# Kernel tuning notes

Hardware: AMD Instinct MI355X
Metric: run time of the kernel (lower is better)

## Reference

```python
import jax, jax.numpy as jnp
import numpy as np

CODEBOOK_SIZE = 8192
DIM = 256
B, T = 8, 4096


def setup_inputs() -> dict:
    key = jax.random.key(0)
    k1, k2, k3 = jax.random.split(key, 3)
    h = jax.random.normal(k1, (B, T, DIM), dtype=jnp.float32)
    mask = jax.random.randint(k2, (B, T), 0, 2).astype(bool)
    codebook = jax.random.normal(k3, (CODEBOOK_SIZE, DIM), dtype=jnp.float32) * 0.02
    return {"h": h, "mask": mask, "codebook": codebook}


def reference(h, mask, codebook):
    Bb, Tt, D = h.shape
    flat = h.reshape(-1, D)  # (N, D)
    # squared euclidean distances (N, K)
    h2 = jnp.sum(flat * flat, axis=-1, keepdims=True)
    c2 = jnp.sum(codebook * codebook, axis=-1)
    dist = h2 + c2 - 2.0 * flat @ codebook.T
    indices = jnp.argmin(dist, axis=-1)  # (N,)
    z = codebook[indices].reshape(Bb, Tt, D)
    m = mask.astype(h.dtype)[:, :, None]  # (B, T, 1)
    denom = jnp.sum(m) * D + 1e-8
    commit_loss = jnp.sum((h - jax.lax.stop_gradient(z)) ** 2 * m) / denom
    codebook_loss = jnp.sum((jax.lax.stop_gradient(h) - z) ** 2 * m) / denom
    z_q = h + jax.lax.stop_gradient(z - h)  # straight-through estimator
    return z_q, indices.reshape(Bb, Tt), commit_loss, codebook_loss
```

## Files before the change

kernel.cpp:

```cpp
#include <hip/hip_runtime.h>

#define NPTS   32768
#define DIM    256
#define KCODES 8192
#define TAU    1e-2f
#define NCAP   16384

typedef __attribute__((ext_vector_type(8))) short bf16x8;
typedef __attribute__((ext_vector_type(4))) float f32x4;

__device__ __forceinline__ unsigned short f2bf(float x) {
  unsigned u = __float_as_uint(x);
  unsigned r = (u + 0x7fffu + ((u >> 16) & 1u)) >> 16;
  return (unsigned short)r;
}

__global__ __launch_bounds__(256) void bf16_norms_kernel(
    const float* __restrict__ src, unsigned short* __restrict__ hi,
    float* __restrict__ norms, int* __restrict__ flagcnt) {
  if (flagcnt && blockIdx.x == 0 && threadIdx.x == 0) *flagcnt = 0;
  int row = blockIdx.x * 4 + (threadIdx.x >> 6);
  int lane = threadIdx.x & 63;
  float4 a = reinterpret_cast<const float4*>(src)[row * 64 + lane];
  ushort4 hq;
  hq.x = f2bf(a.x); hq.y = f2bf(a.y); hq.z = f2bf(a.z); hq.w = f2bf(a.w);
  reinterpret_cast<ushort4*>(hi)[row * 64 + lane] = hq;
  float sx = a.x * a.x, sy = a.y * a.y, sz = a.z * a.z, sw = a.w * a.w;
  double s = (double)sx + (double)sy + (double)sz + (double)sw;
#pragma unroll
  for (int m = 32; m; m >>= 1) s += __shfl_xor(s, m, 64);
  if (lane == 0) norms[row] = (float)s;
}

__global__ __launch_bounds__(256) void norms_kernel(const float* __restrict__ src,
                                                    float* __restrict__ dst) {
  int row = blockIdx.x * 4 + (threadIdx.x >> 6);
  int lane = threadIdx.x & 63;
  float4 a = reinterpret_cast<const float4*>(src)[row * 64 + lane];
  float sx = a.x * a.x, sy = a.y * a.y, sz = a.z * a.z, sw = a.w * a.w;
  double s = (double)sx + (double)sy + (double)sz + (double)sw;
#pragma unroll
  for (int m = 32; m; m >>= 1) s += __shfl_xor(s, m, 64);
  if (lane == 0) dst[row] = (float)s;
}

__global__ __launch_bounds__(512, 2) void mfma_argmin_kernel(
    const unsigned short* __restrict__ hh, const unsigned short* __restrict__ chh,
    const float* __restrict__ c2f,
    float* __restrict__ bv, int* __restrict__ bi, float* __restrict__ b2o) {
  __shared__ __align__(16) unsigned short Ps[8192], Cs[8192];
  __shared__ float tb1[128][4], tb2[128][4];
  __shared__ int ti1[128][4];
  const int t = threadIdx.x;
  const int lane = t & 63;
  const int wid = t >> 6;
  const int wrow = wid >> 2;
  const int cgroup = wid & 3;
  const int b = blockIdx.x;
  const int v = (b & 7) * 64 + (b >> 3);
  const int sblk = v >> 8, pblk = v & 255;
  const int p0 = pblk * 128;
  const int cbase = sblk * (KCODES / 2);

  const int strow = t >> 2, stc = t & 3;
  const int ssw = strow & 7;
  const int stbase = strow * 128;
  const int wd0 = stbase + (((stc * 2) ^ ssw) << 4);
  const int wd1 = stbase + (((stc * 2 + 1) ^ ssw) << 4);
  const char* hhc = (const char*)hh;
  const char* chc = (const char*)chh;
  const unsigned poffs = (unsigned)(p0 + strow) * 512u + (unsigned)(stc * 32);
  const unsigned cbb = (unsigned)(cbase + strow) * 512u + (unsigned)(stc * 32);

  const int flane = lane & 15, fch = lane >> 4;
  int coff[2][2];
#pragma unroll
  for (int cr = 0; cr < 2; ++cr) {
    int ar = cgroup * 32 + cr * 16 + flane;
#pragma unroll
    for (int kp = 0; kp < 2; ++kp)
      coff[cr][kp] = ar * 128 + (((kp * 4 + fch) ^ (ar & 7)) << 4);
  }
  int poff[4][2];
#pragma unroll
  for (int pc = 0; pc < 4; ++pc) {
    int br = wrow * 64 + pc * 16 + flane;
#pragma unroll
    for (int kp = 0; kp < 2; ++kp)
      poff[pc][kp] = br * 128 + (((kp * 4 + fch) ^ (br & 7)) << 4);
  }

  float rb1[4], rb2[4];
  int ri1[4];
#pragma unroll
  for (int pc = 0; pc < 4; ++pc) { rb1[pc] = 3.4e38f; rb2[pc] = 3.4e38f; ri1[pc] = 0; }

#pragma unroll 1
  for (int cc = 0; cc < 32; ++cc) {
    f32x4 acc[8];
#pragma unroll
    for (int q = 0; q < 8; ++q) acc[q] = (f32x4){0.f, 0.f, 0.f, 0.f};
    const unsigned ccc = cbb + (unsigned)cc * 65536u;

#pragma unroll
    for (int dd = 0; dd < 4; ++dd) {
      const unsigned kk = (unsigned)(dd * 128);
      uint4 pa = *(const uint4*)(hhc + poffs + kk);
      uint4 pb = *(const uint4*)(hhc + poffs + kk + 16);
      uint4 ca = *(const uint4*)(chc + ccc + kk);
      uint4 cb2 = *(const uint4*)(chc + ccc + kk + 16);
      __syncthreads();
      *(uint4*)((char*)Ps + wd0) = pa;
      *(uint4*)((char*)Ps + wd1) = pb;
      *(uint4*)((char*)Cs + wd0) = ca;
      *(uint4*)((char*)Cs + wd1) = cb2;
      __syncthreads();
      bf16x8 cf[2][2];
#pragma unroll
      for (int cr = 0; cr < 2; ++cr)
#pragma unroll
        for (int kp = 0; kp < 2; ++kp)
          cf[cr][kp] = *(const bf16x8*)((const char*)Cs + coff[cr][kp]);
#pragma unroll
      for (int pc = 0; pc < 4; ++pc) {
        bf16x8 p0f = *(const bf16x8*)((const char*)Ps + poff[pc][0]);
        bf16x8 p1f = *(const bf16x8*)((const char*)Ps + poff[pc][1]);
        acc[pc] = __builtin_amdgcn_mfma_f32_16x16x32_bf16(cf[0][0], p0f, acc[pc], 0, 0, 0);
        acc[pc] = __builtin_amdgcn_mfma_f32_16x16x32_bf16(cf[0][1], p1f, acc[pc], 0, 0, 0);
        acc[4 + pc] = __builtin_amdgcn_mfma_f32_16x16x32_bf16(cf[1][0], p0f, acc[4 + pc], 0, 0, 0);
        acc[4 + pc] = __builtin_amdgcn_mfma_f32_16x16x32_bf16(cf[1][1], p1f, acc[4 + pc], 0, 0, 0);
      }
    }
    const int code0 = cbase + cc * 128 + cgroup * 32 + fch * 4;
    float c2v[2][4];
#pragma unroll
    for (int cr = 0; cr < 2; ++cr)
#pragma unroll
      for (int r = 0; r < 4; ++r)
        c2v[cr][r] = c2f[code0 + cr * 16 + r];
#pragma unroll
    for (int pc = 0; pc < 4; ++pc) {
#pragma unroll
      for (int cr = 0; cr < 2; ++cr)
#pragma unroll
        for (int r = 0; r < 4; ++r) {
          float sv = fmaf(-2.f, acc[cr * 4 + pc][r], c2v[cr][r]);
          if (sv < rb1[pc]) { rb2[pc] = rb1[pc]; rb1[pc] = sv; ri1[pc] = code0 + cr * 16 + r; }
          else if (sv < rb2[pc]) rb2[pc] = sv;
        }
    }
  }
#pragma unroll
  for (int pc = 0; pc < 4; ++pc) {
    float b1 = rb1[pc], b2 = rb2[pc];
    int i1 = ri1[pc];
#pragma unroll
    for (int m = 16; m <= 32; m <<= 1) {
      float ob1 = __shfl_xor(b1, m, 64);
      int oi1 = __shfl_xor(i1, m, 64);
      float ob2 = __shfl_xor(b2, m, 64);
      float loser = fmaxf(b1, ob1);
      float nb2 = fminf(fminf(b2, ob2), loser);
      if (ob1 < b1 || (ob1 == b1 && oi1 < i1)) { b1 = ob1; i1 = oi1; }
      b2 = nb2;
    }
    if (fch == 0) {
      int pl = wrow * 64 + pc * 16 + flane;
      tb1[pl][cgroup] = b1;
      ti1[pl][cgroup] = i1;
      tb2[pl][cgroup] = b2;
    }
  }
  __syncthreads();
  if (t < 128) {
    float b1 = tb1[t][0], b2 = tb2[t][0];
    int i1 = ti1[t][0];
#pragma unroll
    for (int w = 1; w < 4; ++w) {
      float nb1 = tb1[t][w], nb2v = tb2[t][w];
      int ni1 = ti1[t][w];
      float loser = fmaxf(b1, nb1);
      float m2 = fminf(fminf(b2, nb2v), loser);
      if (nb1 < b1 || (nb1 == b1 && ni1 < i1)) { b1 = nb1; i1 = ni1; }
      b2 = m2;
    }
    int p = p0 + t;
    bv[sblk * NPTS + p] = b1;
    bi[sblk * NPTS + p] = i1;
    b2o[sblk * NPTS + p] = b2;
  }
}

__global__ __launch_bounds__(256) void merge_flag_kernel(
    const float* __restrict__ bv, const int* __restrict__ bi,
    const float* __restrict__ b2o, int* __restrict__ idx,
    float* __restrict__ out_idx_f, int* __restrict__ flagcnt,
    int* __restrict__ flaglist) {
  int p = blockIdx.x * 256 + threadIdx.x;
  float b1 = bv[p]; int i1 = bi[p]; float b2 = b2o[p];
  {
    float pb1 = bv[NPTS + p];
    int pi1 = bi[NPTS + p];
    float pb2 = b2o[NPTS + p];
    float loser = fmaxf(b1, pb1);
    float nb2 = fminf(fminf(b2, pb2), loser);
    if (pb1 < b1 || (pb1 == b1 && pi1 < i1)) { b1 = pb1; i1 = pi1; }
    b2 = nb2;
  }
  idx[p] = i1;
  out_idx_f[p] = (float)i1;
  if (b2 - b1 < TAU) { int s = atomicAdd(flagcnt, 1); flaglist[s] = p; }
}

__global__ __launch_bounds__(256) void compact_kernel(
    const float* __restrict__ h, const float* __restrict__ h2f,
    const int* __restrict__ flagcnt, const int* __restrict__ flaglist,
    float* __restrict__ hc, float* __restrict__ h2c) {
  int n0 = *flagcnt;
  int n = n0 > NCAP ? NCAP : n0;
  int npad = (n + 127) & ~127;
  for (int e = blockIdx.x; e < npad; e += gridDim.x) {
    if (e < n) {
      int p = flaglist[e];
      if (threadIdx.x < 64)
        reinterpret_cast<float4*>(hc + (size_t)e * DIM)[threadIdx.x] =
            reinterpret_cast<const float4*>(h + (size_t)p * DIM)[threadIdx.x];
      if (threadIdx.x == 0) h2c[e] = h2f[p];
    } else {
      if (threadIdx.x < 64)
        reinterpret_cast<float4*>(hc + (size_t)e * DIM)[threadIdx.x] =
            make_float4(0.f, 0.f, 0.f, 0.f);
      if (threadIdx.x == 0) h2c[e] = 0.f;
    }
  }
}

__global__ __launch_bounds__(512, 2) void refine_gemm_kernel(
    const float* __restrict__ hc, const float* __restrict__ cb,
    const float* __restrict__ h2c, const float* __restrict__ c2f,
    const int* __restrict__ flagcnt,
    float* __restrict__ bv16, int* __restrict__ bi16) {
  const int n0 = *flagcnt;
  const int n = n0 > NCAP ? NCAP : n0;
  const int slice = blockIdx.x & 15;
  const int pblk = blockIdx.x >> 4;
  if (pblk * 128 >= n) return;
  __shared__ float hs[16][132];
  __shared__ float cs[16][260];
  const int t = threadIdx.x;
  const int ct = t & 31;
  const int pt = t >> 5;
  const int p0 = pblk * 128;
  const int cbase = slice * 512;
  float best[8]; int besti[8]; float h2r[8];
#pragma unroll
  for (int i = 0; i < 8; ++i) {
    best[i] = 3.4e38f; besti[i] = 0;
    h2r[i] = h2c[p0 + pt * 4 + ((i >> 2) << 6) + (i & 3)];
  }
#pragma unroll 1
  for (int cc = 0; cc < 2; ++cc) {
    const int c0 = cbase + cc * 256;
    float dot[8][8];
#pragma unroll
    for (int i = 0; i < 8; ++i)
#pragma unroll
      for (int j = 0; j < 8; ++j) dot[i][j] = 0.f;
#pragma unroll 1
    for (int dd = 0; dd < DIM / 16; ++dd) {
      const int d0 = dd * 16;
      {
        int p = t >> 2, k4 = (t & 3) << 2;
        float4 w = *reinterpret_cast<const float4*>(hc + (size_t)(p0 + p) * DIM + d0 + k4);
        hs[k4 + 0][p] = w.x; hs[k4 + 1][p] = w.y;
        hs[k4 + 2][p] = w.z; hs[k4 + 3][p] = w.w;
      }
#pragma unroll
      for (int l = 0; l < 2; ++l) {
        int F = t + l * 512;
        int c = F >> 2, k4 = (F & 3) << 2;
        float4 w = *reinterpret_cast<const float4*>(cb + (size_t)(c0 + c) * DIM + d0 + k4);
        cs[k4 + 0][c] = w.x; cs[k4 + 1][c] = w.y;
        cs[k4 + 2][c] = w.z; cs[k4 + 3][c] = w.w;
      }
      __syncthreads();
#pragma unroll
      for (int k = 0; k < 16; ++k) {
        float hv[8], cv[8];
        *reinterpret_cast<float4*>(&hv[0]) = *reinterpret_cast<const float4*>(&hs[k][pt * 4]);
        *reinterpret_cast<float4*>(&hv[4]) = *reinterpret_cast<const float4*>(&hs[k][pt * 4 + 64]);
        *reinterpret_cast<float4*>(&cv[0]) = *reinterpret_cast<const float4*>(&cs[k][ct * 4]);
        *reinterpret_cast<float4*>(&cv[4]) = *reinterpret_cast<const float4*>(&cs[k][ct * 4 + 128]);
#pragma unroll
        for (int i = 0; i < 8; ++i)
#pragma unroll
          for (int j = 0; j < 8; ++j) dot[i][j] = fmaf(hv[i], cv[j], dot[i][j]);
      }
      __syncthreads();
    }
#pragma unroll
    for (int j = 0; j < 8; ++j) {
      int cl = c0 + (ct << 2) + ((j >> 2) << 7) + (j & 3);
      float cc2 = c2f[cl];
#pragma unroll
      for (int i = 0; i < 8; ++i) {
        float A = h2r[i] + cc2;
        float s = A - 2.0f * dot[i][j];
        if (s < best[i]) { best[i] = s; besti[i] = cl; }
      }
    }
  }
#pragma unroll
  for (int i = 0; i < 8; ++i) {
    float b1 = best[i]; int i1 = besti[i];
#pragma unroll
    for (int m = 16; m; m >>= 1) {
      float so = __shfl_xor(b1, m, 64);
      int io = __shfl_xor(i1, m, 64);
      if (so < b1 || (so == b1 && io < i1)) { b1 = so; i1 = io; }
    }
    if (ct == 0) {
      int p = p0 + pt * 4 + ((i >> 2) << 6) + (i & 3);
      bv16[slice * NCAP + p] = b1;
      bi16[slice * NCAP + p] = i1;
    }
  }
}

__global__ __launch_bounds__(256) void scatter_kernel(
    const float* __restrict__ bv16, const int* __restrict__ bi16,
    const int* __restrict__ flagcnt, const int* __restrict__ flaglist,
    int* __restrict__ idx, float* __restrict__ out_idx_f) {
  int n0 = *flagcnt;
  int n = n0 > NCAP ? NCAP : n0;
  int e = blockIdx.x * 256 + threadIdx.x;
  if (e >= n) return;
  float b1 = bv16[e];
  int i1 = bi16[e];
#pragma unroll
  for (int s = 1; s < 16; ++s) {
    float nb = bv16[s * NCAP + e];
    int ni = bi16[s * NCAP + e];
    if (nb < b1 || (nb == b1 && ni < i1)) { b1 = nb; i1 = ni; }
  }
  int p = flaglist[e];
  idx[p] = i1;
  out_idx_f[p] = (float)i1;
}

__global__ __launch_bounds__(256) void refine_left_kernel(
    const float* __restrict__ h, const float* __restrict__ cb,
    const float* __restrict__ h2f, const float* __restrict__ c2f,
    const int* __restrict__ flagcnt, const int* __restrict__ flaglist,
    int* __restrict__ idx, float* __restrict__ out_idx_f) {
  __shared__ float hrow[DIM];
  __shared__ float rb[256];
  __shared__ int ri[256];
  const int n = *flagcnt;
  for (int e = NCAP + blockIdx.x; e < n; e += gridDim.x) {
    const int p = flaglist[e];
    __syncthreads();
    if (threadIdx.x < DIM / 4)
      reinterpret_cast<float4*>(hrow)[threadIdx.x] =
          reinterpret_cast<const float4*>(h + (size_t)p * DIM)[threadIdx.x];
    __syncthreads();
    const float h2 = h2f[p];
    float b1 = 3.4e38f;
    int i1 = 0x7fffffff;
    for (int c = threadIdx.x; c < KCODES; c += 256) {
      const float4* crow = reinterpret_cast<const float4*>(cb + (size_t)c * DIM);
      float dot = 0.f;
#pragma unroll 16
      for (int d4 = 0; d4 < DIM / 4; ++d4) {
        float4 cv = crow[d4];
        dot = fmaf(hrow[4 * d4 + 0], cv.x, dot);
        dot = fmaf(hrow[4 * d4 + 1], cv.y, dot);
        dot = fmaf(hrow[4 * d4 + 2], cv.z, dot);
        dot = fmaf(hrow[4 * d4 + 3], cv.w, dot);
      }
      float A = h2 + c2f[c];
      float s = fmaf(-2.f, dot, A);
      if (s < b1) { b1 = s; i1 = c; }
    }
    rb[threadIdx.x] = b1;
    ri[threadIdx.x] = i1;
    __syncthreads();
    for (int step = 128; step; step >>= 1) {
      if (threadIdx.x < step) {
        float ob = rb[threadIdx.x + step];
        int oi = ri[threadIdx.x + step];
        if (ob < rb[threadIdx.x] || (ob == rb[threadIdx.x] && oi < ri[threadIdx.x])) {
          rb[threadIdx.x] = ob;
          ri[threadIdx.x] = oi;
        }
      }
      __syncthreads();
    }
    if (threadIdx.x == 0) { idx[p] = ri[0]; out_idx_f[p] = (float)ri[0]; }
  }
}

__global__ __launch_bounds__(512, 2) void argmin_fp32_kernel(
    const float* __restrict__ h, const float* __restrict__ cb,
    const float* __restrict__ h2f, const float* __restrict__ c2f,
    float* __restrict__ bestval, int* __restrict__ bestidx) {
  __shared__ float hs[16][132];
  __shared__ float cs[16][260];
  const int t = threadIdx.x;
  const int ct = t & 31;
  const int pt = t >> 5;
  const int b = blockIdx.x;
  const int v = (b & 7) * 64 + (b >> 3);
  const int sblk = v >> 8;
  const int pblk = v & 255;
  const int p0 = pblk * 128;
  const int cbase = sblk * (KCODES / 2);
  float best[8]; int besti[8]; float h2r[8];
#pragma unroll
  for (int i = 0; i < 8; ++i) {
    best[i] = 3.4e38f; besti[i] = 0;
    h2r[i] = h2f[p0 + pt * 4 + ((i >> 2) << 6) + (i & 3)];
  }
#pragma unroll 1
  for (int cc = 0; cc < (KCODES / 2) / 256; ++cc) {
    const int c0 = cbase + cc * 256;
    float dot[8][8];
#pragma unroll
    for (int i = 0; i < 8; ++i)
#pragma unroll
      for (int j = 0; j < 8; ++j) dot[i][j] = 0.f;
#pragma unroll 1
    for (int dd = 0; dd < DIM / 16; ++dd) {
      const int d0 = dd * 16;
      {
        int p = t >> 2, k4 = (t & 3) << 2;
        float4 w = *reinterpret_cast<const float4*>(h + (p0 + p) * DIM + d0 + k4);
        hs[k4 + 0][p] = w.x; hs[k4 + 1][p] = w.y;
        hs[k4 + 2][p] = w.z; hs[k4 + 3][p] = w.w;
      }
#pragma unroll
      for (int l = 0; l < 2; ++l) {
        int F = t + l * 512;
        int c = F >> 2, k4 = (F & 3) << 2;
        float4 w = *reinterpret_cast<const float4*>(cb + (c0 + c) * DIM + d0 + k4);
        cs[k4 + 0][c] = w.x; cs[k4 + 1][c] = w.y;
        cs[k4 + 2][c] = w.z; cs[k4 + 3][c] = w.w;
      }
      __syncthreads();
#pragma unroll
      for (int k = 0; k < 16; ++k) {
        float hv[8], cv[8];
        *reinterpret_cast<float4*>(&hv[0]) = *reinterpret_cast<const float4*>(&hs[k][pt * 4]);
        *reinterpret_cast<float4*>(&hv[4]) = *reinterpret_cast<const float4*>(&hs[k][pt * 4 + 64]);
        *reinterpret_cast<float4*>(&cv[0]) = *reinterpret_cast<const float4*>(&cs[k][ct * 4]);
        *reinterpret_cast<float4*>(&cv[4]) = *reinterpret_cast<const float4*>(&cs[k][ct * 4 + 128]);
#pragma unroll
        for (int i = 0; i < 8; ++i)
#pragma unroll
          for (int j = 0; j < 8; ++j) dot[i][j] = fmaf(hv[i], cv[j], dot[i][j]);
      }
      __syncthreads();
    }
#pragma unroll
    for (int j = 0; j < 8; ++j) {
      int cl = c0 + (ct << 2) + ((j >> 2) << 7) + (j & 3);
      float cc2 = c2f[cl];
#pragma unroll
      for (int i = 0; i < 8; ++i) {
        float A = h2r[i] + cc2;
        float s = A - 2.0f * dot[i][j];
        if (s < best[i]) { best[i] = s; besti[i] = cl; }
      }
    }
  }
#pragma unroll
  for (int i = 0; i < 8; ++i) {
    float b1 = best[i]; int i1 = besti[i];
#pragma unroll
    for (int m = 16; m; m >>= 1) {
      float so = __shfl_xor(b1, m, 64);
      int io = __shfl_xor(i1, m, 64);
      if (so < b1 || (so == b1 && io < i1)) { b1 = so; i1 = io; }
    }
    if (ct == 0) {
      int p = p0 + pt * 4 + ((i >> 2) << 6) + (i & 3);
      bestval[sblk * NPTS + p] = b1;
      bestidx[sblk * NPTS + p] = i1;
    }
  }
}

__global__ __launch_bounds__(256) void merge2_kernel(
    const float* __restrict__ bestval, const int* __restrict__ bestidx,
    int* __restrict__ idx, float* __restrict__ out_idx_f) {
  int p = blockIdx.x * 256 + threadIdx.x;
  float v0 = bestval[p], v1 = bestval[NPTS + p];
  int i0 = bestidx[p], i1 = bestidx[NPTS + p];
  int w = (v1 < v0) ? i1 : i0;
  idx[p] = w;
  out_idx_f[p] = (float)w;
}

__global__ __launch_bounds__(256) void gather_kernel(
    const float* __restrict__ h, const float* __restrict__ cb,
    const unsigned char* __restrict__ maskb, const int* __restrict__ idx,
    float* __restrict__ zq, float* __restrict__ partial) {
  int p = blockIdx.x * 4 + (threadIdx.x >> 6);
  int lane = threadIdx.x & 63;
  int ci = idx[p];
  float4 hv = reinterpret_cast<const float4*>(h)[p * (DIM / 4) + lane];
  float4 zv = reinterpret_cast<const float4*>(cb)[ci * (DIM / 4) + lane];
  float4 q;
  q.x = hv.x + (zv.x - hv.x);
  q.y = hv.y + (zv.y - hv.y);
  q.z = hv.z + (zv.z - hv.z);
  q.w = hv.w + (zv.w - hv.w);
  reinterpret_cast<float4*>(zq)[p * (DIM / 4) + lane] = q;
  float dx = hv.x - zv.x, dy = hv.y - zv.y, dz = hv.z - zv.z, dw = hv.w - zv.w;
  float s = (maskb[p] != 0) ? (dx * dx + dy * dy + dz * dz + dw * dw) : 0.f;
#pragma unroll
  for (int m = 32; m; m >>= 1) s += __shfl_xor(s, m, 64);
  __shared__ float bs[4];
  if (lane == 0) bs[threadIdx.x >> 6] = s;
  __syncthreads();
  if (threadIdx.x == 0) partial[blockIdx.x] = bs[0] + bs[1] + bs[2] + bs[3];
}

__global__ __launch_bounds__(256) void finalize_kernel(
    const float* __restrict__ partial, const unsigned char* __restrict__ maskb,
    float* __restrict__ out_losses) {
  __shared__ float red[256];
  __shared__ int redi[256];
  float s = 0.f;
  for (int i = threadIdx.x; i < NPTS / 4; i += 256) s += partial[i];
  int cnt = 0;
  for (int i = threadIdx.x; i < NPTS; i += 256) cnt += (maskb[i] != 0);
  red[threadIdx.x] = s;
  redi[threadIdx.x] = cnt;
  __syncthreads();
  for (int step = 128; step; step >>= 1) {
    if (threadIdx.x < step) {
      red[threadIdx.x] += red[threadIdx.x + step];
      redi[threadIdx.x] += redi[threadIdx.x + step];
    }
    __syncthreads();
  }
  if (threadIdx.x == 0) {
    float denom = (float)redi[0] * (float)DIM + 1e-8f;
    float loss = red[0] / denom;
    out_losses[0] = loss;
    out_losses[1] = loss;
  }
}

extern "C" void kernel_launch(void* const* d_in, const int* in_sizes, int n_in,
                              void* d_out, int out_size, void* d_ws, size_t ws_size,
                              hipStream_t stream) {
  const float* h = (const float*)d_in[0];
  const unsigned char* maskb = (const unsigned char*)d_in[1];
  const float* cb = (const float*)d_in[2];

  float* out = (float*)d_out;
  float* zq = out;
  float* out_idx_f = out + NPTS * DIM;
  float* out_losses = out + NPTS * DIM + NPTS;

  char* ws = (char*)d_ws;
  const size_t REQ = 42008576ULL;

  if (ws_size >= REQ) {
    float* h2f = (float*)(ws + 0);
    float* c2f = (float*)(ws + 131072);
    float* bv = (float*)(ws + 163840);
    int* bi = (int*)(ws + 688128);
    float* b2o = (float*)(ws + 1212416);
    int* idx = (int*)(ws + 1736704);
    float* partial = (float*)(ws + 1867776);
    int* flagcnt = (int*)(ws + 1900544);
    int* flaglist = (int*)(ws + 1904640);
    unsigned short* hh = (unsigned short*)(ws + 2097152);
    unsigned short* chh = (unsigned short*)(ws + 18874368);
    float* hcomp = (float*)(ws + 23068672);
    float* h2comp = (float*)(ws + 39845888);
    float* bv16 = (float*)(ws + 39911424);
    int* bi16 = (int*)(ws + 40960000);

    hipLaunchKernelGGL(bf16_norms_kernel, dim3(NPTS / 4), dim3(256), 0, stream,
                       h, hh, h2f, flagcnt);
    hipLaunchKernelGGL(bf16_norms_kernel, dim3(KCODES / 4), dim3(256), 0, stream,
                       cb, chh, c2f, (int*)nullptr);
    hipLaunchKernelGGL(mfma_argmin_kernel, dim3(512), dim3(512), 0, stream,
                       hh, chh, c2f, bv, bi, b2o);
    hipLaunchKernelGGL(merge_flag_kernel, dim3(NPTS / 256), dim3(256), 0, stream,
                       bv, bi, b2o, idx, out_idx_f, flagcnt, flaglist);
    hipLaunchKernelGGL(compact_kernel, dim3(2048), dim3(256), 0, stream,
                       h, h2f, flagcnt, flaglist, hcomp, h2comp);
    hipLaunchKernelGGL(refine_gemm_kernel, dim3((NCAP / 128) * 16), dim3(512), 0, stream,
                       hcomp, cb, h2comp, c2f, flagcnt, bv16, bi16);
    hipLaunchKernelGGL(scatter_kernel, dim3(NCAP / 256), dim3(256), 0, stream,
                       bv16, bi16, flagcnt, flaglist, idx, out_idx_f);
    hipLaunchKernelGGL(refine_left_kernel, dim3(2048), dim3(256), 0, stream,
                       h, cb, h2f, c2f, flagcnt, flaglist, idx, out_idx_f);
    hipLaunchKernelGGL(gather_kernel, dim3(NPTS / 4), dim3(256), 0, stream,
                       h, cb, maskb, idx, zq, partial);
    hipLaunchKernelGGL(finalize_kernel, dim3(1), dim3(256), 0, stream,
                       partial, maskb, out_losses);
  } else {
    float* h2f = (float*)(ws + 0);
    float* c2f = (float*)(ws + (128 << 10));
    float* bestval = (float*)(ws + (160 << 10));
    int* bestidx = (int*)(ws + (416 << 10));
    int* idx = (int*)(ws + (672 << 10));
    float* partial = (float*)(ws + (800 << 10));

    hipLaunchKernelGGL(norms_kernel, dim3(NPTS / 4), dim3(256), 0, stream, h, h2f);
    hipLaunchKernelGGL(norms_kernel, dim3(KCODES / 4), dim3(256), 0, stream, cb, c2f);
    hipLaunchKernelGGL(argmin_fp32_kernel, dim3(512), dim3(512), 0, stream,
                       h, cb, h2f, c2f, bestval, bestidx);
    hipLaunchKernelGGL(merge2_kernel, dim3(NPTS / 256), dim3(256), 0, stream,
                       bestval, bestidx, idx, out_idx_f);
    hipLaunchKernelGGL(gather_kernel, dim3(NPTS / 4), dim3(256), 0, stream,
                       h, cb, maskb, idx, zq, partial);
    hipLaunchKernelGGL(finalize_kernel, dim3(1), dim3(256), 0, stream,
                       partial, maskb, out_losses);
  }
}
```

Measured before the change: 397.9 us.

## Replace fp32 refine GEMM with bf16 MFMA candidate collection plus exact rescoring

Ambiguous points were previously refined by a full fp32 GEMM against all codes. They now get a bf16 MFMA pass that gathers up to 32 candidate codes within a margin of the bf16 best, and each candidate is then rescored exactly in fp32. Points that overflow the candidate list fall back to the exhaustive refine_left path. This removes the fp32 SIMT GEMM and the compaction copy. It adds per-candidate atomics and relies on the margin being large enough to cover bf16 error, which is a correctness risk.

```diff
diff --git a/kernel.cpp b/kernel.cpp
--- a/kernel.cpp
+++ b/kernel.cpp
@@ -4,6 +4,7 @@
 #define DIM    256
 #define KCODES 8192
 #define TAU    1e-2f
+#define TAU2   3e-2f
 #define NCAP   16384
 
 typedef __attribute__((ext_vector_type(8))) short bf16x8;
@@ -195,7 +196,8 @@
     const float* __restrict__ bv, const int* __restrict__ bi,
     const float* __restrict__ b2o, int* __restrict__ idx,
     float* __restrict__ out_idx_f, int* __restrict__ flagcnt,
-    int* __restrict__ flaglist) {
+    int* __restrict__ flaglist, float* __restrict__ bminc,
+    int* __restrict__ cnt) {
   int p = blockIdx.x * 256 + threadIdx.x;
   float b1 = bv[p]; int i1 = bi[p]; float b2 = b2o[p];
   {
@@ -209,155 +211,200 @@
   }
   idx[p] = i1;
   out_idx_f[p] = (float)i1;
-  if (b2 - b1 < TAU) { int s = atomicAdd(flagcnt, 1); flaglist[s] = p; }
-}
-
-__global__ __launch_bounds__(256) void compact_kernel(
-    const float* __restrict__ h, const float* __restrict__ h2f,
+  if (b2 - b1 < TAU) {
+    int s = atomicAdd(flagcnt, 1);
+    flaglist[s] = p;
+    if (s < NCAP) { bminc[s] = b1; cnt[s] = 0; }
+  }
+}
+
+__global__ __launch_bounds__(512, 2) void collect_kernel(
+    const unsigned short* __restrict__ hh, const unsigned short* __restrict__ chh,
+    const float* __restrict__ c2f, const int* __restrict__ flagcnt,
+    const int* __restrict__ flaglist, const float* __restrict__ bminc,
+    int* __restrict__ cnt, int* __restrict__ cand) {
+  __shared__ __align__(16) unsigned short Ps[8192], Cs[8192];
+  const int n0 = *flagcnt;
+  const int n = n0 > NCAP ? NCAP : n0;
+  const int pblk = blockIdx.x >> 1;
+  const int sblk = blockIdx.x & 1;
+  const int p0c = pblk * 128;
+  if (p0c >= n) return;
+  const int t = threadIdx.x;
+  const int lane = t & 63;
+  const int wid = t >> 6;
+  const int wrow = wid >> 2;
+  const int cgroup = wid & 3;
+  const int cbase = sblk * (KCODES / 2);
+
+  const int strow = t >> 2, stc = t & 3;
+  const int ssw = strow & 7;
+  const int stbase = strow * 128;
+  const int wd0 = stbase + (((stc * 2) ^ ssw) << 4);
+  const int wd1 = stbase + (((stc * 2 + 1) ^ ssw) << 4);
+  const char* hhc = (const char*)hh;
+  const char* chc = (const char*)chh;
+  const int prow_e = p0c + strow;
+  const int prow = (prow_e < n) ? flaglist[prow_e] : flaglist[0];
+  const unsigned poffs = (unsigned)prow * 512u + (unsigned)(stc * 32);
+  const unsigned cbb = (unsigned)(cbase + strow) * 512u + (unsigned)(stc * 32);
+
+  const int flane = lane & 15, fch = lane >> 4;
+  int coff[2][2];
+#pragma unroll
+  for (int cr = 0; cr < 2; ++cr) {
+    int ar = cgroup * 32 + cr * 16 + flane;
+#pragma unroll
+    for (int kp = 0; kp < 2; ++kp)
+      coff[cr][kp] = ar * 128 + (((kp * 4 + fch) ^ (ar & 7)) << 4);
+  }
+  int poff[4][2];
+#pragma unroll
+  for (int pc = 0; pc < 4; ++pc) {
+    int br = wrow * 64 + pc * 16 + flane;
+#pragma unroll
+    for (int kp = 0; kp < 2; ++kp)
+      poff[pc][kp] = br * 128 + (((kp * 4 + fch) ^ (br & 7)) << 4);
+  }
+
+  int ept[4];
+  float thr[4];
+#pragma unroll
+  for (int pc = 0; pc < 4; ++pc) {
+    int e = p0c + wrow * 64 + pc * 16 + flane;
+    ept[pc] = e;
+    thr[pc] = (e < n) ? (bminc[e] + TAU2) : -3.4e38f;
+  }
+
+#pragma unroll 1
+  for (int cc = 0; cc < 32; ++cc) {
+    f32x4 acc[8];
+#pragma unroll
+    for (int q = 0; q < 8; ++q) acc[q] = (f32x4){0.f, 0.f, 0.f, 0.f};
+    const unsigned ccc = cbb + (unsigned)cc * 65536u;
+
+#pragma unroll
+    for (int dd = 0; dd < 4; ++dd) {
+      const unsigned kk = (unsigned)(dd * 128);
+      uint4 pa = *(const uint4*)(hhc + poffs + kk);
+      uint4 pb = *(const uint4*)(hhc + poffs + kk + 16);
+      uint4 ca = *(const uint4*)(chc + ccc + kk);
+      uint4 cb2 = *(const uint4*)(chc + ccc + kk + 16);
+      __syncthreads();
+      *(uint4*)((char*)Ps + wd0) = pa;
+      *(uint4*)((char*)Ps + wd1) = pb;
+      *(uint4*)((char*)Cs + wd0) = ca;
+      *(uint4*)((char*)Cs + wd1) = cb2;
+      __syncthreads();
+      bf16x8 cf[2][2];
+#pragma unroll
+      for (int cr = 0; cr < 2; ++cr)
+#pragma unroll
+        for (int kp = 0; kp < 2; ++kp)
+          cf[cr][kp] = *(const bf16x8*)((const char*)Cs + coff[cr][kp]);
+#pragma unroll
+      for (int pc = 0; pc < 4; ++pc) {
+        bf16x8 p0f = *(const bf16x8*)((const char*)Ps + poff[pc][0]);
+        bf16x8 p1f = *(const bf16x8*)((const char*)Ps + poff[pc][1]);
+        acc[pc] = __builtin_amdgcn_mfma_f32_16x16x32_bf16(cf[0][0], p0f, acc[pc], 0, 0, 0);
+        acc[pc] = __builtin_amdgcn_mfma_f32_16x16x32_bf16(cf[0][1], p1f, acc[pc], 0, 0, 0);
+        acc[4 + pc] = __builtin_amdgcn_mfma_f32_16x16x32_bf16(cf[1][0], p0f, acc[4 + pc], 0, 0, 0);
+        acc[4 + pc] = __builtin_amdgcn_mfma_f32_16x16x32_bf16(cf[1][1], p1f, acc[4 + pc], 0, 0, 0);
+      }
+    }
+    const int code0 = cbase + cc * 128 + cgroup * 32 + fch * 4;
+    float c2v[2][4];
+#pragma unroll
+    for (int cr = 0; cr < 2; ++cr)
+#pragma unroll
+      for (int r = 0; r < 4; ++r)
+        c2v[cr][r] = c2f[code0 + cr * 16 + r];
+#pragma unroll
+    for (int pc = 0; pc < 4; ++pc) {
+#pragma unroll
+      for (int cr = 0; cr < 2; ++cr)
+#pragma unroll
+        for (int r = 0; r < 4; ++r) {
+          float sv = fmaf(-2.f, acc[cr * 4 + pc][r], c2v[cr][r]);
+          if (sv < thr[pc]) {
+            int slot = atomicAdd(&cnt[ept[pc]], 1);
+            if (slot < 32) cand[ept[pc] * 32 + slot] = code0 + cr * 16 + r;
+          }
+        }
+    }
+  }
+}
+
+__global__ __launch_bounds__(256) void cand_exact_kernel(
+    const float* __restrict__ h, const float* __restrict__ cb,
+    const float* __restrict__ h2f, const float* __restrict__ c2f,
     const int* __restrict__ flagcnt, const int* __restrict__ flaglist,
-    float* __restrict__ hc, float* __restrict__ h2c) {
-  int n0 = *flagcnt;
-  int n = n0 > NCAP ? NCAP : n0;
-  int npad = (n + 127) & ~127;
-  for (int e = blockIdx.x; e < npad; e += gridDim.x) {
+    const int* __restrict__ cnt, const int* __restrict__ cand,
+    int* __restrict__ idx, float* __restrict__ out_idx_f) {
+  __shared__ float hrows[8][DIM];
+  const int n0 = *flagcnt;
+  const int n = n0 > NCAP ? NCAP : n0;
+  const int e0 = blockIdx.x * 8;
+  if (e0 >= n) return;
+  for (int i = threadIdx.x; i < 8 * 64; i += 256) {
+    int rr = i >> 6;
+    int e = e0 + rr;
     if (e < n) {
       int p = flaglist[e];
-      if (threadIdx.x < 64)
-        reinterpret_cast<float4*>(hc + (size_t)e * DIM)[threadIdx.x] =
-            reinterpret_cast<const float4*>(h + (size_t)p * DIM)[threadIdx.x];
-      if (threadIdx.x == 0) h2c[e] = h2f[p];
-    } else {
-      if (threadIdx.x < 64)
-        reinterpret_cast<float4*>(hc + (size_t)e * DIM)[threadIdx.x] =
-            make_float4(0.f, 0.f, 0.f, 0.f);
-      if (threadIdx.x == 0) h2c[e] = 0.f;
-    }
-  }
-}
-
-__global__ __launch_bounds__(512, 2) void refine_gemm_kernel(
-    const float* __restrict__ hc, const float* __restrict__ cb,
-    const float* __restrict__ h2c, const float* __restrict__ c2f,
-    const int* __restrict__ flagcnt,
-    float* __restrict__ bv16, int* __restrict__ bi16) {
-  const int n0 = *flagcnt;
-  const int n = n0 > NCAP ? NCAP : n0;
-  const int slice = blockIdx.x & 15;
-  const int pblk = blockIdx.x >> 4;
-  if (pblk * 128 >= n) return;
-  __shared__ float hs[16][132];
-  __shared__ float cs[16][260];
-  const int t = threadIdx.x;
-  const int ct = t & 31;
-  const int pt = t >> 5;
-  const int p0 = pblk * 128;
-  const int cbase = slice * 512;
-  float best[8]; int besti[8]; float h2r[8];
-#pragma unroll
-  for (int i = 0; i < 8; ++i) {
-    best[i] = 3.4e38f; besti[i] = 0;
-    h2r[i] = h2c[p0 + pt * 4 + ((i >> 2) << 6) + (i & 3)];
-  }
-#pragma unroll 1
-  for (int cc = 0; cc < 2; ++cc) {
-    const int c0 = cbase + cc * 256;
-    float dot[8][8];
-#pragma unroll
-    for (int i = 0; i < 8; ++i)
-#pragma unroll
-      for (int j = 0; j < 8; ++j) dot[i][j] = 0.f;
-#pragma unroll 1
-    for (int dd = 0; dd < DIM / 16; ++dd) {
-      const int d0 = dd * 16;
-      {
-        int p = t >> 2, k4 = (t & 3) << 2;
-        float4 w = *reinterpret_cast<const float4*>(hc + (size_t)(p0 + p) * DIM + d0 + k4);
-        hs[k4 + 0][p] = w.x; hs[k4 + 1][p] = w.y;
-        hs[k4 + 2][p] = w.z; hs[k4 + 3][p] = w.w;
-      }
-#pragma unroll
-      for (int l = 0; l < 2; ++l) {
-        int F = t + l * 512;
-        int c = F >> 2, k4 = (F & 3) << 2;
-        float4 w = *reinterpret_cast<const float4*>(cb + (size_t)(c0 + c) * DIM + d0 + k4);
-        cs[k4 + 0][c] = w.x; cs[k4 + 1][c] = w.y;
-        cs[k4 + 2][c] = w.z; cs[k4 + 3][c] = w.w;
-      }
-      __syncthreads();
-#pragma unroll
-      for (int k = 0; k < 16; ++k) {
-        float hv[8], cv[8];
-        *reinterpret_cast<float4*>(&hv[0]) = *reinterpret_cast<const float4*>(&hs[k][pt * 4]);
-        *reinterpret_cast<float4*>(&hv[4]) = *reinterpret_cast<const float4*>(&hs[k][pt * 4 + 64]);
-        *reinterpret_cast<float4*>(&cv[0]) = *reinterpret_cast<const float4*>(&cs[k][ct * 4]);
-        *reinterpret_cast<float4*>(&cv[4]) = *reinterpret_cast<const float4*>(&cs[k][ct * 4 + 128]);
-#pragma unroll
-        for (int i = 0; i < 8; ++i)
-#pragma unroll
-          for (int j = 0; j < 8; ++j) dot[i][j] = fmaf(hv[i], cv[j], dot[i][j]);
-      }
-      __syncthreads();
-    }
-#pragma unroll
-    for (int j = 0; j < 8; ++j) {
-      int cl = c0 + (ct << 2) + ((j >> 2) << 7) + (j & 3);
-      float cc2 = c2f[cl];
-#pragma unroll
-      for (int i = 0; i < 8; ++i) {
-        float A = h2r[i] + cc2;
-        float s = A - 2.0f * dot[i][j];
-        if (s < best[i]) { best[i] = s; besti[i] = cl; }
-      }
-    }
-  }
-#pragma unroll
-  for (int i = 0; i < 8; ++i) {
-    float b1 = best[i]; int i1 = besti[i];
-#pragma unroll
-    for (int m = 16; m; m >>= 1) {
-      float so = __shfl_xor(b1, m, 64);
-      int io = __shfl_xor(i1, m, 64);
-      if (so < b1 || (so == b1 && io < i1)) { b1 = so; i1 = io; }
-    }
-    if (ct == 0) {
-      int p = p0 + pt * 4 + ((i >> 2) << 6) + (i & 3);
-      bv16[slice * NCAP + p] = b1;
-      bi16[slice * NCAP + p] = i1;
-    }
-  }
-}
-
-__global__ __launch_bounds__(256) void scatter_kernel(
-    const float* __restrict__ bv16, const int* __restrict__ bi16,
-    const int* __restrict__ flagcnt, const int* __restrict__ flaglist,
-    int* __restrict__ idx, float* __restrict__ out_idx_f) {
-  int n0 = *flagcnt;
-  int n = n0 > NCAP ? NCAP : n0;
-  int e = blockIdx.x * 256 + threadIdx.x;
-  if (e >= n) return;
-  float b1 = bv16[e];
-  int i1 = bi16[e];
-#pragma unroll
-  for (int s = 1; s < 16; ++s) {
-    float nb = bv16[s * NCAP + e];
-    int ni = bi16[s * NCAP + e];
-    if (nb < b1 || (nb == b1 && ni < i1)) { b1 = nb; i1 = ni; }
-  }
-  int p = flaglist[e];
-  idx[p] = i1;
-  out_idx_f[p] = (float)i1;
+      reinterpret_cast<float4*>(hrows[rr])[i & 63] =
+          reinterpret_cast<const float4*>(h + (size_t)p * DIM)[i & 63];
+    }
+  }
+  __syncthreads();
+  const int rr = threadIdx.x >> 5;
+  const int slot = threadIdx.x & 31;
+  const int e = e0 + rr;
+  float best = 3.4e38f;
+  int besti = 0x7fffffff;
+  bool valid = (e < n) && (cnt[e] <= 32);
+  if (valid && slot < cnt[e]) {
+    int c = cand[e * 32 + slot];
+    const float4* crow = reinterpret_cast<const float4*>(cb + (size_t)c * DIM);
+    const float* hr = hrows[rr];
+    float dot = 0.f;
+#pragma unroll 16
+    for (int q = 0; q < DIM / 4; ++q) {
+      float4 cv = crow[q];
+      dot = fmaf(hr[4 * q + 0], cv.x, dot);
+      dot = fmaf(hr[4 * q + 1], cv.y, dot);
+      dot = fmaf(hr[4 * q + 2], cv.z, dot);
+      dot = fmaf(hr[4 * q + 3], cv.w, dot);
+    }
+    float A = h2f[flaglist[e]] + c2f[c];
+    best = fmaf(-2.f, dot, A);
+    besti = c;
+  }
+#pragma unroll
+  for (int m = 1; m <= 16; m <<= 1) {
+    float ob = __shfl_xor(best, m, 32);
+    int oi = __shfl_xor(besti, m, 32);
+    if (ob < best || (ob == best && oi < besti)) { best = ob; besti = oi; }
+  }
+  if (valid && slot == 0) {
+    int p = flaglist[e];
+    idx[p] = besti;
+    out_idx_f[p] = (float)besti;
+  }
 }
 
 __global__ __launch_bounds__(256) void refine_left_kernel(
     const float* __restrict__ h, const float* __restrict__ cb,
     const float* __restrict__ h2f, const float* __restrict__ c2f,
     const int* __restrict__ flagcnt, const int* __restrict__ flaglist,
+    const int* __restrict__ cnt,
     int* __restrict__ idx, float* __restrict__ out_idx_f) {
   __shared__ float hrow[DIM];
   __shared__ float rb[256];
   __shared__ int ri[256];
-  const int n = *flagcnt;
-  for (int e = NCAP + blockIdx.x; e < n; e += gridDim.x) {
+  const int ntot = *flagcnt;
+  for (int e = blockIdx.x; e < ntot; e += gridDim.x) {
+    bool needs = (e >= NCAP) || (cnt[e] > 32);
+    if (!needs) continue;
     const int p = flaglist[e];
     __syncthreads();
     if (threadIdx.x < DIM / 4)
@@ -566,24 +613,23 @@
   float* out_losses = out + NPTS * DIM + NPTS;
 
   char* ws = (char*)d_ws;
-  const size_t REQ = 42008576ULL;
+  const size_t REQ = 25165824ULL;
 
   if (ws_size >= REQ) {
     float* h2f = (float*)(ws + 0);
     float* c2f = (float*)(ws + 131072);
     float* bv = (float*)(ws + 163840);
-    int* bi = (int*)(ws + 688128);
-    float* b2o = (float*)(ws + 1212416);
-    int* idx = (int*)(ws + 1736704);
-    float* partial = (float*)(ws + 1867776);
-    int* flagcnt = (int*)(ws + 1900544);
-    int* flaglist = (int*)(ws + 1904640);
-    unsigned short* hh = (unsigned short*)(ws + 2097152);
-    unsigned short* chh = (unsigned short*)(ws + 18874368);
-    float* hcomp = (float*)(ws + 23068672);
-    float* h2comp = (float*)(ws + 39845888);
-    float* bv16 = (float*)(ws + 39911424);
-    int* bi16 = (int*)(ws + 40960000);
+    int* bi = (int*)(ws + 425984);
+    float* b2o = (float*)(ws + 688128);
+    float* bminc = (float*)(ws + 950272);
+    int* idx = (int*)(ws + 1015808);
+    float* partial = (float*)(ws + 1146880);
+    int* flagcnt = (int*)(ws + 1179648);
+    int* flaglist = (int*)(ws + 1183744);
+    int* cnt = (int*)(ws + 1314816);
+    int* cand = (int*)(ws + 1380352);
+    unsigned short* hh = (unsigned short*)(ws + 4194304);
+    unsigned short* chh = (unsigned short*)(ws + 20971520);
 
     hipLaunchKernelGGL(bf16_norms_kernel, dim3(NPTS / 4), dim3(256), 0, stream,
                        h, hh, h2f, flagcnt);
@@ -592,15 +638,13 @@
     hipLaunchKernelGGL(mfma_argmin_kernel, dim3(512), dim3(512), 0, stream,
                        hh, chh, c2f, bv, bi, b2o);
     hipLaunchKernelGGL(merge_flag_kernel, dim3(NPTS / 256), dim3(256), 0, stream,
-                       bv, bi, b2o, idx, out_idx_f, flagcnt, flaglist);
-    hipLaunchKernelGGL(compact_kernel, dim3(2048), dim3(256), 0, stream,
-                       h, h2f, flagcnt, flaglist, hcomp, h2comp);
-    hipLaunchKernelGGL(refine_gemm_kernel, dim3((NCAP / 128) * 16), dim3(512), 0, stream,
-                       hcomp, cb, h2comp, c2f, flagcnt, bv16, bi16);
-    hipLaunchKernelGGL(scatter_kernel, dim3(NCAP / 256), dim3(256), 0, stream,
-                       bv16, bi16, flagcnt, flaglist, idx, out_idx_f);
+                       bv, bi, b2o, idx, out_idx_f, flagcnt, flaglist, bminc, cnt);
+    hipLaunchKernelGGL(collect_kernel, dim3((NCAP / 128) * 2), dim3(512), 0, stream,
+                       hh, chh, c2f, flagcnt, flaglist, bminc, cnt, cand);
+    hipLaunchKernelGGL(cand_exact_kernel, dim3(NCAP / 8), dim3(256), 0, stream,
+                       h, cb, h2f, c2f, flagcnt, flaglist, cnt, cand, idx, out_idx_f);
     hipLaunchKernelGGL(refine_left_kernel, dim3(2048), dim3(256), 0, stream,
-                       h, cb, h2f, c2f, flagcnt, flaglist, idx, out_idx_f);
+                       h, cb, h2f, c2f, flagcnt, flaglist, cnt, idx, out_idx_f);
     hipLaunchKernelGGL(gather_kernel, dim3(NPTS / 4), dim3(256), 0, stream,
                        h, cb, maskb, idx, zq, partial);
     hipLaunchKernelGGL(finalize_kernel, dim3(1), dim3(256), 0, stream,
```

Measured after the change: 409.8 us. 1.03x slower.
